# Performance work log

Measured on AMD Instinct MI355X. Metric: run time of the kernel, lower is better.

The kernel has to match this reference:

```python
import jax, jax.numpy as jnp
import numpy as np

N_NODES = 50000
N_EDGES = 1600000
IN_DIM = 128
HID = [128, 128]
OUT_DIM = 64
N_USERS = 10000


def setup_inputs() -> dict:
    key = jax.random.key(0)
    ks = jax.random.split(key, 12)
    features = jax.random.normal(ks[0], (N_NODES, IN_DIM), jnp.float32)
    src = jax.random.randint(ks[1], (N_EDGES,), 0, N_NODES)
    dst = jax.random.randint(ks[2], (N_EDGES,), 0, N_NODES)
    users = jax.random.randint(ks[3], (N_USERS,), 0, N_NODES)
    s = 0.05
    W0 = jax.random.normal(ks[4], (IN_DIM, HID[0]), jnp.float32) * s
    b0 = jnp.zeros((HID[0],), jnp.float32)
    W1 = jax.random.normal(ks[5], (HID[0], HID[1]), jnp.float32) * s
    b1 = jnp.zeros((HID[1],), jnp.float32)
    Ws1 = jax.random.normal(ks[6], (HID[1], 64), jnp.float32) * s
    bs1 = jnp.zeros((64,), jnp.float32)
    Ws2 = jax.random.normal(ks[7], (64, OUT_DIM), jnp.float32) * s
    bs2 = jnp.zeros((OUT_DIM,), jnp.float32)
    return {"features": features, "W0": W0, "b0": b0, "W1": W1, "b1": b1,
            "Ws1": Ws1, "bs1": bs1, "Ws2": Ws2, "bs2": bs2,
            "src": src, "dst": dst, "users": users}


def _gcn_layer(h, src, dst, cs, cd, W, b):
    # DGL GraphConv, norm='both': relu(D_in^-1/2 A D_out^-1/2 (h W) + b)
    h = h @ W                                   # [N, d_out]
    m = (h * cs)[src]                           # [E, d_out] gathered messages
    agg = jax.ops.segment_sum(m, dst, num_segments=N_NODES)
    return jax.nn.relu(agg * cd + b)


def reference(features, W0, b0, W1, b1, Ws1, bs1, Ws2, bs2, src, dst, users):
    ones = jnp.ones(src.shape[0], jnp.float32)
    deg_out = jax.ops.segment_sum(ones, src, num_segments=N_NODES)
    deg_in = jax.ops.segment_sum(ones, dst, num_segments=N_NODES)
    cs = jnp.maximum(deg_out, 1.0)[:, None] ** -0.5  # source-side norm
    cd = jnp.maximum(deg_in, 1.0)[:, None] ** -0.5   # dest-side norm
    h = _gcn_layer(features, src, dst, cs, cd, W0, b0)
    # dropout between layers: identity in eval mode
    h = _gcn_layer(h, src, dst, cs, cd, W1, b1)
    user_h = h[users]                            # [U, HID[-1]]
    R = jnp.tanh(user_h @ Ws1 + bs1) @ Ws2 + bs2  # SR head
    return (R, h)
```

## Files before the change

### kernel.cpp

```cpp
#include <hip/hip_runtime.h>
#include <hip/hip_bf16.h>
#include <hip/hip_fp16.h>

#define NN 50000
#define NE 1600000
#define DIM 128
#define NU 10000
#define NB 256
#define SLICE_W 12500
#define NE4 (NE / 4)
#define CHUNK4 ((NE4 + NB - 1) / NB)
#define NRB 98

__global__ __launch_bounds__(1024) void k_hist(const int4* __restrict__ src4,
                                               const int4* __restrict__ dst4,
                                               unsigned int* __restrict__ histD,
                                               unsigned int* __restrict__ histS) {
    __shared__ unsigned int lh[SLICE_W];
    for (int i = threadIdx.x; i < SLICE_W; i += 1024) lh[i] = 0u;
    __syncthreads();
    int b = blockIdx.x & (NB - 1);
    const int4* idx4 = (blockIdx.x < NB) ? dst4 : src4;
    unsigned int* out = ((blockIdx.x < NB) ? histD : histS) + (size_t)b * SLICE_W;
    int beg = b * CHUNK4, end = min(beg + CHUNK4, NE4);
    for (int i = beg + threadIdx.x; i < end; i += 1024) {
        int4 v = idx4[i];
        atomicAdd(&lh[v.x >> 2], 1u << ((v.x & 3) * 8));
        atomicAdd(&lh[v.y >> 2], 1u << ((v.y & 3) * 8));
        atomicAdd(&lh[v.z >> 2], 1u << ((v.z & 3) * 8));
        atomicAdd(&lh[v.w >> 2], 1u << ((v.w & 3) * 8));
    }
    __syncthreads();
    for (int i = threadIdx.x; i < SLICE_W; i += 1024) out[i] = lh[i];
}

__global__ __launch_bounds__(256) void k_reduce_norms(const unsigned int* __restrict__ histD,
                                                      const unsigned int* __restrict__ histS,
                                                      int* __restrict__ din,
                                                      float* __restrict__ cs, float* __restrict__ cd,
                                                      int* __restrict__ partials) {
    __shared__ unsigned int part8[128][8];
    __shared__ int red[256];
    int wl = threadIdx.x & 127;
    int g = threadIdx.x >> 7;
    int wi = blockIdx.x * 128 + wl;
    unsigned int d0 = 0, d1 = 0, d2 = 0, d3 = 0, s0 = 0, s1 = 0, s2 = 0, s3 = 0;
    if (wi < SLICE_W) {
        for (int b = g * 128; b < g * 128 + 128; ++b) {
            unsigned int wd = histD[(size_t)b * SLICE_W + wi];
            unsigned int ws = histS[(size_t)b * SLICE_W + wi];
            d0 += wd & 0xFFu; d1 += (wd >> 8) & 0xFFu; d2 += (wd >> 16) & 0xFFu; d3 += wd >> 24;
            s0 += ws & 0xFFu; s1 += (ws >> 8) & 0xFFu; s2 += (ws >> 16) & 0xFFu; s3 += ws >> 24;
        }
    }
    red[threadIdx.x] = (int)(d0 + d1 + d2 + d3);
    if (g == 1) {
        part8[wl][0] = d0; part8[wl][1] = d1; part8[wl][2] = d2; part8[wl][3] = d3;
        part8[wl][4] = s0; part8[wl][5] = s1; part8[wl][6] = s2; part8[wl][7] = s3;
    }
    __syncthreads();
    if (g == 0 && wi < SLICE_W) {
        d0 += part8[wl][0]; d1 += part8[wl][1]; d2 += part8[wl][2]; d3 += part8[wl][3];
        s0 += part8[wl][4]; s1 += part8[wl][5]; s2 += part8[wl][6]; s3 += part8[wl][7];
        int n = wi * 4;
        *(int4*)&din[n] = make_int4(d0, d1, d2, d3);
        float4 vcd, vcs;
        vcd.x = rsqrtf(fmaxf((float)d0, 1.f)); vcd.y = rsqrtf(fmaxf((float)d1, 1.f));
        vcd.z = rsqrtf(fmaxf((float)d2, 1.f)); vcd.w = rsqrtf(fmaxf((float)d3, 1.f));
        vcs.x = rsqrtf(fmaxf((float)s0, 1.f)); vcs.y = rsqrtf(fmaxf((float)s1, 1.f));
        vcs.z = rsqrtf(fmaxf((float)s2, 1.f)); vcs.w = rsqrtf(fmaxf((float)s3, 1.f));
        *(float4*)&cd[n] = vcd;
        *(float4*)&cs[n] = vcs;
    }
    for (int off = 128; off > 0; off >>= 1) {
        if (threadIdx.x < off) red[threadIdx.x] += red[threadIdx.x + off];
        __syncthreads();
    }
    if (threadIdx.x == 0) partials[blockIdx.x] = red[0];
}

__global__ __launch_bounds__(64) void k_scan2(const int* __restrict__ partials,
                                              int* __restrict__ bases) {
    int lane = threadIdx.x;
    int p0 = (2 * lane < NRB) ? partials[2 * lane] : 0;
    int p1 = (2 * lane + 1 < NRB) ? partials[2 * lane + 1] : 0;
    int pair = p0 + p1;
    int s = pair;
    for (int off = 1; off < 64; off <<= 1) {
        int n = __shfl_up(s, off);
        if (lane >= off) s += n;
    }
    int excl = s - pair;
    if (2 * lane < NRB) bases[2 * lane] = excl;
    if (2 * lane + 1 < NRB) bases[2 * lane + 1] = excl + p0;
}

__global__ __launch_bounds__(128) void k_scan3(const int* __restrict__ din,
                                               const int* __restrict__ bases,
                                               int* __restrict__ offs) {
    __shared__ int part[128];
    int t = threadIdx.x;
    int n0 = blockIdx.x * 512 + t * 4;
    int4 d = make_int4(0, 0, 0, 0);
    if (n0 < NN) d = *(const int4*)&din[n0];
    int tsum = d.x + d.y + d.z + d.w;
    part[t] = tsum;
    __syncthreads();
    for (int off = 1; off < 128; off <<= 1) {
        int v = (t >= off) ? part[t - off] : 0;
        __syncthreads();
        part[t] += v;
        __syncthreads();
    }
    if (n0 < NN) {
        int o = bases[blockIdx.x] + part[t] - tsum;
        *(int4*)&offs[n0] = make_int4(o, o + d.x, o + d.x + d.y, o + d.x + d.y + d.z);
    }
}

__global__ __launch_bounds__(256) void k_blockbase(const unsigned int* __restrict__ histD,
                                                   unsigned char* __restrict__ rel8) {
    int n = blockIdx.x * blockDim.x + threadIdx.x;
    if (n >= NN) return;
    int wi = n >> 2, sh = (n & 3) * 8;
    unsigned int run = 0;
    for (int b = 0; b < NB; ++b) {
        rel8[(size_t)b * NN + n] = (unsigned char)run;
        run += (histD[(size_t)b * SLICE_W + wi] >> sh) & 0xFFu;
    }
}

__global__ __launch_bounds__(1024) void k_scatter2(const int4* __restrict__ src4,
                                                   const int4* __restrict__ dst4,
                                                   const int* __restrict__ offs,
                                                   const unsigned char* __restrict__ rel8,
                                                   unsigned short* __restrict__ csc) {
    __shared__ unsigned int lc[SLICE_W];
    for (int i = threadIdx.x; i < SLICE_W; i += 1024) lc[i] = 0u;
    __syncthreads();
    int b = blockIdx.x;
    const unsigned char* rel = rel8 + (size_t)b * NN;
    int beg = b * CHUNK4, end = min(beg + CHUNK4, NE4);
    for (int i = beg + threadIdx.x; i < end; i += 1024) {
        int4 s = src4[i];
        int4 d = dst4[i];
#pragma unroll
        for (int j = 0; j < 4; ++j) {
            int dd = (j == 0) ? d.x : (j == 1) ? d.y : (j == 2) ? d.z : d.w;
            int ss = (j == 0) ? s.x : (j == 1) ? s.y : (j == 2) ? s.z : s.w;
            int sh = (dd & 3) * 8;
            unsigned int old = atomicAdd(&lc[dd >> 2], 1u << sh);
            int local = (old >> sh) & 0xFF;
            csc[offs[dd] + rel[dd] + local] = (unsigned short)ss;
        }
    }
}

__global__ __launch_bounds__(256) void k_matmul_cs(const float* __restrict__ X,
                                                   const float* __restrict__ W,
                                                   const float* __restrict__ cs,
                                                   __half* __restrict__ Y, int nrows) {
    __shared__ __half sW[DIM * DIM];
    __shared__ float sX[16][DIM];
    for (int i = threadIdx.x * 4; i < DIM * DIM; i += 256 * 4) {
        float4 w4 = *(const float4*)&W[i];
        *(__half2*)&sW[i]     = __float22half2_rn(make_float2(w4.x, w4.y));
        *(__half2*)&sW[i + 2] = __float22half2_rn(make_float2(w4.z, w4.w));
    }
    int rl = threadIdx.x >> 6;
    int c = (threadIdx.x & 63) * 2;
    int ngroups = (nrows + 15) >> 4;
    for (int g = blockIdx.x; g < ngroups; g += gridDim.x) {
        __syncthreads();
        {
            int row = threadIdx.x >> 4;
            int col = (threadIdx.x & 15) * 8;
            int rr = min(g * 16 + row, nrows - 1);
            const float* xp = X + (size_t)rr * DIM + col;
            *(float4*)&sX[row][col] = *(const float4*)xp;
            *(float4*)&sX[row][col + 4] = *(const float4*)(xp + 4);
        }
        __syncthreads();
        float acc[4][2] = {};
#pragma unroll 4
        for (int k = 0; k < DIM; ++k) {
            float2 w = __half22float2(*(const __half2*)&sW[k * DIM + c]);
            float x0 = sX[rl * 4 + 0][k];
            float x1 = sX[rl * 4 + 1][k];
            float x2 = sX[rl * 4 + 2][k];
            float x3 = sX[rl * 4 + 3][k];
            acc[0][0] = fmaf(x0, w.x, acc[0][0]); acc[0][1] = fmaf(x0, w.y, acc[0][1]);
            acc[1][0] = fmaf(x1, w.x, acc[1][0]); acc[1][1] = fmaf(x1, w.y, acc[1][1]);
            acc[2][0] = fmaf(x2, w.x, acc[2][0]); acc[2][1] = fmaf(x2, w.y, acc[2][1]);
            acc[3][0] = fmaf(x3, w.x, acc[3][0]); acc[3][1] = fmaf(x3, w.y, acc[3][1]);
        }
#pragma unroll
        for (int j = 0; j < 4; ++j) {
            int r = g * 16 + rl * 4 + j;
            if (r < nrows) {
                float s = cs[r];
                __half2 hv = __float22half2_rn(make_float2(acc[j][0] * s, acc[j][1] * s));
                *(__half2*)&Y[(size_t)r * DIM + c] = hv;
            }
        }
    }
}

__global__ __launch_bounds__(256) void k_aggregate(const __half* __restrict__ hs,
                                                   const unsigned short* __restrict__ csc,
                                                   const int* __restrict__ offs,
                                                   const int* __restrict__ din,
                                                   const float* __restrict__ cd,
                                                   const float* __restrict__ bias,
                                                   float* __restrict__ out) {
    int wid = threadIdx.x >> 6;
    int lane = threadIdx.x & 63;
    int h = lane >> 5;
    int l = lane & 31;
    int d = blockIdx.x * 4 + wid;
    int beg = offs[d];
    int end = beg + din[d];
    const __half* base = hs + l * 4;
    float a0 = 0.f, a1 = 0.f, a2 = 0.f, a3 = 0.f;
    float b0 = 0.f, b1 = 0.f, b2 = 0.f, b3 = 0.f;
    float c0 = 0.f, c1 = 0.f, c2 = 0.f, c3 = 0.f;
    float e0 = 0.f, e1 = 0.f, e2 = 0.f, e3 = 0.f;
    int i = beg + h;
    for (; i + 14 < end; i += 16) {
        int sI[8];
#pragma unroll
        for (int j = 0; j < 8; ++j) sI[j] = csc[i + 2 * j];
        short4 vI[8];
#pragma unroll
        for (int j = 0; j < 8; ++j) vI[j] = *(const short4*)(base + (size_t)sI[j] * DIM);
#pragma unroll
        for (int j = 0; j < 8; j += 4) {
            float2 x0 = __half22float2(*(const __half2*)&vI[j].x);
            float2 x1 = __half22float2(*(const __half2*)&vI[j].z);
            float2 y0 = __half22float2(*(const __half2*)&vI[j + 1].x);
            float2 y1 = __half22float2(*(const __half2*)&vI[j + 1].z);
            float2 z0 = __half22float2(*(const __half2*)&vI[j + 2].x);
            float2 z1 = __half22float2(*(const __half2*)&vI[j + 2].z);
            float2 w0 = __half22float2(*(const __half2*)&vI[j + 3].x);
            float2 w1 = __half22float2(*(const __half2*)&vI[j + 3].z);
            a0 += x0.x; a1 += x0.y; a2 += x1.x; a3 += x1.y;
            b0 += y0.x; b1 += y0.y; b2 += y1.x; b3 += y1.y;
            c0 += z0.x; c1 += z0.y; c2 += z1.x; c3 += z1.y;
            e0 += w0.x; e1 += w0.y; e2 += w1.x; e3 += w1.y;
        }
    }
    for (; i + 6 < end; i += 8) {
        int s0 = csc[i], s1 = csc[i + 2], s2 = csc[i + 4], s3 = csc[i + 6];
        short4 v0 = *(const short4*)(base + (size_t)s0 * DIM);
        short4 v1 = *(const short4*)(base + (size_t)s1 * DIM);
        short4 v2 = *(const short4*)(base + (size_t)s2 * DIM);
        short4 v3 = *(const short4*)(base + (size_t)s3 * DIM);
        float2 x0 = __half22float2(*(const __half2*)&v0.x);
        float2 x1 = __half22float2(*(const __half2*)&v0.z);
        float2 y0 = __half22float2(*(const __half2*)&v1.x);
        float2 y1 = __half22float2(*(const __half2*)&v1.z);
        float2 z0 = __half22float2(*(const __half2*)&v2.x);
        float2 z1 = __half22float2(*(const __half2*)&v2.z);
        float2 w0 = __half22float2(*(const __half2*)&v3.x);
        float2 w1 = __half22float2(*(const __half2*)&v3.z);
        a0 += x0.x; a1 += x0.y; a2 += x1.x; a3 += x1.y;
        b0 += y0.x; b1 += y0.y; b2 += y1.x; b3 += y1.y;
        c0 += z0.x; c1 += z0.y; c2 += z1.x; c3 += z1.y;
        e0 += w0.x; e1 += w0.y; e2 += w1.x; e3 += w1.y;
    }
    for (; i < end; i += 2) {
        int s = csc[i];
        short4 v = *(const short4*)(base + (size_t)s * DIM);
        float2 x0 = __half22float2(*(const __half2*)&v.x);
        float2 x1 = __half22float2(*(const __half2*)&v.z);
        a0 += x0.x; a1 += x0.y; a2 += x1.x; a3 += x1.y;
    }
    a0 += b0 + c0 + e0; a1 += b1 + c1 + e1;
    a2 += b2 + c2 + e2; a3 += b3 + c3 + e3;
    a0 += __shfl(a0, lane ^ 32);
    a1 += __shfl(a1, lane ^ 32);
    a2 += __shfl(a2, lane ^ 32);
    a3 += __shfl(a3, lane ^ 32);
    if (h == 0) {
        float c = cd[d];
        float4 bv = *(const float4*)&bias[l * 4];
        float4 o;
        o.x = fmaxf(fmaf(a0, c, bv.x), 0.f);
        o.y = fmaxf(fmaf(a1, c, bv.y), 0.f);
        o.z = fmaxf(fmaf(a2, c, bv.z), 0.f);
        o.w = fmaxf(fmaf(a3, c, bv.w), 0.f);
        *(float4*)&out[(size_t)d * DIM + l * 4] = o;
    }
}

__global__ __launch_bounds__(256) void k_sr_head(const float* __restrict__ h,
                                                 const int* __restrict__ users,
                                                 const float* __restrict__ Ws1,
                                                 const float* __restrict__ bs1,
                                                 const float* __restrict__ Ws2,
                                                 const float* __restrict__ bs2,
                                                 float* __restrict__ R, int nu) {
    __shared__ float sW1[DIM * 64];
    __shared__ float sW2[64 * 64];
    __shared__ float sU[4][DIM];
    __shared__ float sT[4][64];
    for (int i = threadIdx.x * 4; i < DIM * 64; i += 256 * 4)
        *(float4*)&sW1[i] = *(const float4*)&Ws1[i];
    for (int i = threadIdx.x * 4; i < 64 * 64; i += 256 * 4)
        *(float4*)&sW2[i] = *(const float4*)&Ws2[i];
    int ul = threadIdx.x >> 6;
    int c = threadIdx.x & 63;
    for (int base = blockIdx.x * 4; base < nu; base += gridDim.x * 4) {
        int u = base + ul;
        __syncthreads();
        if (u < nu) {
            int node = users[u];
            *(float2*)&sU[ul][c * 2] = *(const float2*)&h[(size_t)node * DIM + c * 2];
        }
        __syncthreads();
        float t = 0.f;
        if (u < nu) {
            float acc = bs1[c];
#pragma unroll 8
            for (int k = 0; k < DIM; ++k) acc = fmaf(sU[ul][k], sW1[k * 64 + c], acc);
            t = tanhf(acc);
        }
        sT[ul][c] = t;
        __syncthreads();
        if (u < nu) {
            float acc = bs2[c];
#pragma unroll 8
            for (int k = 0; k < 64; ++k) acc = fmaf(sT[ul][k], sW2[k * 64 + c], acc);
            R[(size_t)u * 64 + c] = acc;
        }
    }
}

extern "C" void kernel_launch(void* const* d_in, const int* in_sizes, int n_in,
                              void* d_out, int out_size, void* d_ws, size_t ws_size,
                              hipStream_t stream) {
    const float* features = (const float*)d_in[0];
    const float* W0  = (const float*)d_in[1];
    const float* b0  = (const float*)d_in[2];
    const float* W1  = (const float*)d_in[3];
    const float* b1  = (const float*)d_in[4];
    const float* Ws1 = (const float*)d_in[5];
    const float* bs1 = (const float*)d_in[6];
    const float* Ws2 = (const float*)d_in[7];
    const float* bs2 = (const float*)d_in[8];
    const int* src   = (const int*)d_in[9];
    const int* dst   = (const int*)d_in[10];
    const int* users = (const int*)d_in[11];

    float* R = (float*)d_out;
    float* H = (float*)d_out + (size_t)NU * 64;

    char* ws = (char*)d_ws;
    __half* hsA  = (__half*)(ws + 0);
    unsigned int* histD = (unsigned int*)(ws + 0);
    unsigned int* histS = (unsigned int*)(ws + 12800000);
    unsigned char* rel8 = (unsigned char*)(ws + 12800000);
    unsigned short* csc = (unsigned short*)(ws + 25600000);
    int*   din   = (int*)  (ws + 28800000);
    float* cs    = (float*)(ws + 29000000);
    float* cd    = (float*)(ws + 29200000);
    int*   offs  = (int*)  (ws + 29400000);
    int*   partials = (int*)(ws + 29600000);
    int*   bases    = (int*)(ws + 29601024);

    k_hist<<<2 * NB, 1024, 0, stream>>>((const int4*)src, (const int4*)dst, histD, histS);
    k_reduce_norms<<<NRB, 256, 0, stream>>>(histD, histS, din, cs, cd, partials);
    k_scan2<<<1, 64, 0, stream>>>(partials, bases);
    k_scan3<<<NRB, 128, 0, stream>>>(din, bases, offs);
    k_blockbase<<<(NN + 255) / 256, 256, 0, stream>>>(histD, rel8);
    k_scatter2<<<NB, 1024, 0, stream>>>((const int4*)src, (const int4*)dst, offs, rel8, csc);

    k_matmul_cs<<<1024, 256, 0, stream>>>(features, W0, cs, hsA, NN);
    k_aggregate<<<12500, 256, 0, stream>>>(hsA, csc, offs, din, cd, b0, H);

    k_matmul_cs<<<1024, 256, 0, stream>>>(H, W1, cs, hsA, NN);
    k_aggregate<<<12500, 256, 0, stream>>>(hsA, csc, offs, din, cd, b1, H);

    k_sr_head<<<625, 256, 0, stream>>>(H, users, Ws1, bs1, Ws2, bs2, R, NU);
}
```

Measured before the change: 285.2 us.

## Use MFMA f16 matrix cores for dense transform and fold block-base scan into scan3

Replaces the scalar-FMA fp16-weight matmul with a kernel that packs X and W into 16x16x32 f16 MFMA fragments in shared memory. Each wave computes a 16-row tile across all 128 output columns, which is meant to move the dense transform onto the matrix cores. Separately, the single-block k_scan2 launch is removed, and each k_scan3 block now reduces the preceding partials itself, saving one kernel launch. The risks are fp16 rounding of X inputs (previously kept in fp32), scattered 2-byte output stores, and redundant partial reductions per block.

```diff
diff --git a/kernel.cpp b/kernel.cpp
--- a/kernel.cpp
+++ b/kernel.cpp
@@ -11,6 +11,10 @@
 #define NE4 (NE / 4)
 #define CHUNK4 ((NE4 + NB - 1) / NB)
 #define NRB 98
+#define MM_ROWS 64
+
+typedef __attribute__((ext_vector_type(8))) _Float16 f16x8;
+typedef __attribute__((ext_vector_type(4))) float f32x4;
 
 __global__ __launch_bounds__(1024) void k_hist(const int4* __restrict__ src4,
                                                const int4* __restrict__ dst4,
@@ -79,31 +83,26 @@
     if (threadIdx.x == 0) partials[blockIdx.x] = red[0];
 }
 
-__global__ __launch_bounds__(64) void k_scan2(const int* __restrict__ partials,
-                                              int* __restrict__ bases) {
-    int lane = threadIdx.x;
-    int p0 = (2 * lane < NRB) ? partials[2 * lane] : 0;
-    int p1 = (2 * lane + 1 < NRB) ? partials[2 * lane + 1] : 0;
-    int pair = p0 + p1;
-    int s = pair;
-    for (int off = 1; off < 64; off <<= 1) {
-        int n = __shfl_up(s, off);
-        if (lane >= off) s += n;
-    }
-    int excl = s - pair;
-    if (2 * lane < NRB) bases[2 * lane] = excl;
-    if (2 * lane + 1 < NRB) bases[2 * lane + 1] = excl + p0;
-}
-
 __global__ __launch_bounds__(128) void k_scan3(const int* __restrict__ din,
-                                               const int* __restrict__ bases,
+                                               const int* __restrict__ partials,
                                                int* __restrict__ offs) {
     __shared__ int part[128];
+    __shared__ int sbase;
     int t = threadIdx.x;
+    part[t] = (t < blockIdx.x) ? partials[t] : 0;
+    __syncthreads();
+    for (int off = 64; off > 0; off >>= 1) {
+        if (t < off) part[t] += part[t + off];
+        __syncthreads();
+    }
+    if (t == 0) sbase = part[0];
+    __syncthreads();
+    int base = sbase;
     int n0 = blockIdx.x * 512 + t * 4;
     int4 d = make_int4(0, 0, 0, 0);
     if (n0 < NN) d = *(const int4*)&din[n0];
     int tsum = d.x + d.y + d.z + d.w;
+    __syncthreads();
     part[t] = tsum;
     __syncthreads();
     for (int off = 1; off < 128; off <<= 1) {
@@ -113,7 +112,7 @@
         __syncthreads();
     }
     if (n0 < NN) {
-        int o = bases[blockIdx.x] + part[t] - tsum;
+        int o = base + part[t] - tsum;
         *(int4*)&offs[n0] = make_int4(o, o + d.x, o + d.x + d.y, o + d.x + d.y + d.z);
     }
 }
@@ -156,51 +155,67 @@
     }
 }
 
-__global__ __launch_bounds__(256) void k_matmul_cs(const float* __restrict__ X,
-                                                   const float* __restrict__ W,
-                                                   const float* __restrict__ cs,
-                                                   __half* __restrict__ Y, int nrows) {
-    __shared__ __half sW[DIM * DIM];
-    __shared__ float sX[16][DIM];
-    for (int i = threadIdx.x * 4; i < DIM * DIM; i += 256 * 4) {
-        float4 w4 = *(const float4*)&W[i];
-        *(__half2*)&sW[i]     = __float22half2_rn(make_float2(w4.x, w4.y));
-        *(__half2*)&sW[i + 2] = __float22half2_rn(make_float2(w4.z, w4.w));
-    }
-    int rl = threadIdx.x >> 6;
-    int c = (threadIdx.x & 63) * 2;
-    int ngroups = (nrows + 15) >> 4;
-    for (int g = blockIdx.x; g < ngroups; g += gridDim.x) {
-        __syncthreads();
-        {
-            int row = threadIdx.x >> 4;
-            int col = (threadIdx.x & 15) * 8;
-            int rr = min(g * 16 + row, nrows - 1);
-            const float* xp = X + (size_t)rr * DIM + col;
-            *(float4*)&sX[row][col] = *(const float4*)xp;
-            *(float4*)&sX[row][col + 4] = *(const float4*)(xp + 4);
-        }
-        __syncthreads();
-        float acc[4][2] = {};
-#pragma unroll 4
-        for (int k = 0; k < DIM; ++k) {
-            float2 w = __half22float2(*(const __half2*)&sW[k * DIM + c]);
-            float x0 = sX[rl * 4 + 0][k];
-            float x1 = sX[rl * 4 + 1][k];
-            float x2 = sX[rl * 4 + 2][k];
-            float x3 = sX[rl * 4 + 3][k];
-            acc[0][0] = fmaf(x0, w.x, acc[0][0]); acc[0][1] = fmaf(x0, w.y, acc[0][1]);
-            acc[1][0] = fmaf(x1, w.x, acc[1][0]); acc[1][1] = fmaf(x1, w.y, acc[1][1]);
-            acc[2][0] = fmaf(x2, w.x, acc[2][0]); acc[2][1] = fmaf(x2, w.y, acc[2][1]);
-            acc[3][0] = fmaf(x3, w.x, acc[3][0]); acc[3][1] = fmaf(x3, w.y, acc[3][1]);
-        }
-#pragma unroll
-        for (int j = 0; j < 4; ++j) {
-            int r = g * 16 + rl * 4 + j;
-            if (r < nrows) {
-                float s = cs[r];
-                __half2 hv = __float22half2_rn(make_float2(acc[j][0] * s, acc[j][1] * s));
-                *(__half2*)&Y[(size_t)r * DIM + c] = hv;
+__global__ __launch_bounds__(256) void k_matmul_mfma(const float* __restrict__ X,
+                                                     const float* __restrict__ W,
+                                                     const float* __restrict__ cs,
+                                                     __half* __restrict__ Y, int nrows) {
+    __shared__ f16x8 sB[8][4][64];
+    __shared__ f16x8 sA[4][4][64];
+    int t = threadIdx.x;
+    for (int e = t; e < 8 * 4 * 64; e += 256) {
+        int ct = e >> 8;
+        int k0 = (e >> 6) & 3;
+        int l = e & 63;
+        int c = ct * 16 + (l & 15);
+        int kb = k0 * 32 + ((l >> 4) << 3);
+        f16x8 frag;
+#pragma unroll
+        for (int j = 0; j < 8; ++j) frag[j] = (_Float16)W[(size_t)(kb + j) * DIM + c];
+        sB[ct][k0][l] = frag;
+    }
+    int wave = t >> 6;
+    int l = t & 63;
+    int crow = (l >> 4) * 4;
+    int ccol = l & 15;
+    int ng = (nrows + MM_ROWS - 1) / MM_ROWS;
+    for (int g = blockIdx.x; g < ng; g += gridDim.x) {
+        int rbase = g * MM_ROWS;
+        __syncthreads();
+        for (int e = t; e < 4 * 4 * 64; e += 256) {
+            int wt = e >> 8;
+            int k0 = (e >> 6) & 3;
+            int ll = e & 63;
+            int r = min(rbase + wt * 16 + (ll & 15), nrows - 1);
+            int kb = k0 * 32 + ((ll >> 4) << 3);
+            const float* xp = X + (size_t)r * DIM + kb;
+            float4 xa = *(const float4*)xp;
+            float4 xb = *(const float4*)(xp + 4);
+            f16x8 frag;
+            frag[0] = (_Float16)xa.x; frag[1] = (_Float16)xa.y;
+            frag[2] = (_Float16)xa.z; frag[3] = (_Float16)xa.w;
+            frag[4] = (_Float16)xb.x; frag[5] = (_Float16)xb.y;
+            frag[6] = (_Float16)xb.z; frag[7] = (_Float16)xb.w;
+            sA[wt][k0][ll] = frag;
+        }
+        __syncthreads();
+        f16x8 a0 = sA[wave][0][l], a1 = sA[wave][1][l];
+        f16x8 a2 = sA[wave][2][l], a3 = sA[wave][3][l];
+        float csv[4];
+#pragma unroll
+        for (int j = 0; j < 4; ++j)
+            csv[j] = cs[min(rbase + wave * 16 + crow + j, nrows - 1)];
+#pragma unroll
+        for (int ct = 0; ct < 8; ++ct) {
+            f32x4 acc = {0.f, 0.f, 0.f, 0.f};
+            acc = __builtin_amdgcn_mfma_f32_16x16x32_f16(a0, sB[ct][0][l], acc, 0, 0, 0);
+            acc = __builtin_amdgcn_mfma_f32_16x16x32_f16(a1, sB[ct][1][l], acc, 0, 0, 0);
+            acc = __builtin_amdgcn_mfma_f32_16x16x32_f16(a2, sB[ct][2][l], acc, 0, 0, 0);
+            acc = __builtin_amdgcn_mfma_f32_16x16x32_f16(a3, sB[ct][3][l], acc, 0, 0, 0);
+#pragma unroll
+            for (int j = 0; j < 4; ++j) {
+                int r = rbase + wave * 16 + crow + j;
+                if (r < nrows)
+                    Y[(size_t)r * DIM + ct * 16 + ccol] = __float2half(acc[j] * csv[j]);
             }
         }
     }
@@ -366,19 +381,17 @@
     float* cd    = (float*)(ws + 29200000);
     int*   offs  = (int*)  (ws + 29400000);
     int*   partials = (int*)(ws + 29600000);
-    int*   bases    = (int*)(ws + 29601024);
 
     k_hist<<<2 * NB, 1024, 0, stream>>>((const int4*)src, (const int4*)dst, histD, histS);
     k_reduce_norms<<<NRB, 256, 0, stream>>>(histD, histS, din, cs, cd, partials);
-    k_scan2<<<1, 64, 0, stream>>>(partials, bases);
-    k_scan3<<<NRB, 128, 0, stream>>>(din, bases, offs);
+    k_scan3<<<NRB, 128, 0, stream>>>(din, partials, offs);
     k_blockbase<<<(NN + 255) / 256, 256, 0, stream>>>(histD, rel8);
     k_scatter2<<<NB, 1024, 0, stream>>>((const int4*)src, (const int4*)dst, offs, rel8, csc);
 
-    k_matmul_cs<<<1024, 256, 0, stream>>>(features, W0, cs, hsA, NN);
+    k_matmul_mfma<<<782, 256, 0, stream>>>(features, W0, cs, hsA, NN);
     k_aggregate<<<12500, 256, 0, stream>>>(hsA, csc, offs, din, cd, b0, H);
 
-    k_matmul_cs<<<1024, 256, 0, stream>>>(H, W1, cs, hsA, NN);
+    k_matmul_mfma<<<782, 256, 0, stream>>>(H, W1, cs, hsA, NN);
     k_aggregate<<<12500, 256, 0, stream>>>(hsA, csc, offs, din, cd, b1, H);
 
     k_sr_head<<<625, 256, 0, stream>>>(H, users, Ws1, bs1, Ws2, bs2, R, NU);
```

Measured after the change: 247.0 us, median of 2. -13.4%, faster.
